# Optimization experiments

Hardware: AMD Instinct MI355X
Metric: run time of the kernel (lower is better)

The kernel has to match this reference:

```python
import jax, jax.numpy as jnp
import numpy as np

EMBED_DIM = 1024
NUM_HEADS = 16
SEQ = 2048
BATCH = 2


def setup_inputs() -> dict:
    key = jax.random.key(0)
    ks = jax.random.split(key, 9)
    E = EMBED_DIM
    gain = 1.0 / np.sqrt(2.0)  # xavier_uniform with gain 1/sqrt(2) (qkv_same_dim)
    limit = gain * np.sqrt(6.0 / (E + E))
    q = jax.random.normal(ks[0], (SEQ, BATCH, E), dtype=jnp.float32)
    k = jax.random.normal(ks[1], (SEQ, BATCH, E), dtype=jnp.float32)
    v = jax.random.normal(ks[2], (SEQ, BATCH, E), dtype=jnp.float32)
    Wq = jax.random.uniform(ks[3], (E, E), jnp.float32, -limit, limit)
    Wk = jax.random.uniform(ks[4], (E, E), jnp.float32, -limit, limit)
    Wv = jax.random.uniform(ks[5], (E, E), jnp.float32, -limit, limit)
    bq = jnp.zeros((E,), jnp.float32)
    bk = jnp.zeros((E,), jnp.float32)
    bv = jnp.zeros((E,), jnp.float32)
    return {"query": q, "key": k, "value": v,
            "Wq": Wq, "bq": bq, "Wk": Wk, "bk": bk, "Wv": Wv, "bv": bv}


def reference(query, key, value, Wq, bq, Wk, bk, Wv, bv):
    # Base Taylor attention path (norm_taylor=True, do_scale=True, has_out=False).
    L, B, E = query.shape
    H = NUM_HEADS
    hd = E // H
    scaling = E ** (-0.5)  # self.scaling = dim**-0.5, dim == embed_dim

    q = (query @ Wq + bq) * scaling          # (L, B, E)
    k = key @ Wk + bk                         # (S, B, E)
    v = value @ Wv + bv                       # (S, B, E)

    def split_heads(x):
        # (T, B, E) -> (B*H, T, hd)
        T = x.shape[0]
        return x.reshape(T, B * H, hd).transpose(1, 0, 2)

    qh, kh, vh = split_heads(q), split_heads(k), split_heads(v)

    # Taylor expansion of exp(qk) to first order: 1 + q.k
    attn = 1.0 + jnp.einsum('bld,bsd->bls', qh, kh)   # (B*H, L, S)
    attn = attn / attn.sum(axis=-1, keepdims=True)    # row-normalize
    out = jnp.einsum('bls,bsd->bld', attn, vh)        # (B*H, L, hd)
    out = out.transpose(1, 0, 2).reshape(L, B, E)     # (L, B, E)
    return out
```

## Files before the change

kernel.cpp:

```cpp
#include <hip/hip_runtime.h>
#include <hip/hip_bf16.h>

#define L_SEQ 2048
#define BATCH 2
#define ROWS 4096
#define E 1024
#define NH 16
#define HD 64

typedef __attribute__((ext_vector_type(4))) float f32x4;
typedef __attribute__((ext_vector_type(8))) __bf16 bf16x8;

#define SWZ(byt) ((byt) ^ ((((byt) >> 7) & 7) << 4))

__device__ __forceinline__ void gload16(const void* g, void* l) {
    __builtin_amdgcn_global_load_lds((const __attribute__((address_space(1))) void*)g,
                                     (__attribute__((address_space(3))) void*)l,
                                     16, 0, 0);
}

__global__ __launch_bounds__(256) void prep(const float* __restrict__ q,
                                            const float* __restrict__ k,
                                            const float* __restrict__ v,
                                            const float* __restrict__ Wq,
                                            const float* __restrict__ Wk,
                                            const float* __restrict__ Wv,
                                            __bf16* __restrict__ Xb,
                                            __bf16* __restrict__ Wt) {
    const int z = blockIdx.y;
    if (blockIdx.x < 2048) {
        const float* src = (z == 0) ? q : ((z == 1) ? k : v);
        __bf16* dst = Xb + (size_t)z * ROWS * E;
        const size_t i = ((size_t)blockIdx.x * 256 + threadIdx.x) * 8;
        const float4 a = *(const float4*)(src + i);
        const float4 b = *(const float4*)(src + i + 4);
        bf16x8 o;
        o[0] = (__bf16)a.x; o[1] = (__bf16)a.y; o[2] = (__bf16)a.z; o[3] = (__bf16)a.w;
        o[4] = (__bf16)b.x; o[5] = (__bf16)b.y; o[6] = (__bf16)b.z; o[7] = (__bf16)b.w;
        *(bf16x8*)(dst + i) = o;
        return;
    }
    const float* W = (z == 0) ? Wq : ((z == 1) ? Wk : Wv);
    __bf16* dst = Wt + (size_t)z * E * E;
    __shared__ __align__(16) float t[64][65];
    const int tt = blockIdx.x - 2048;
    const int n0 = (tt & 15) * 64, k0 = (tt >> 4) * 64;
    const int r = threadIdx.x >> 2, c4 = threadIdx.x & 3;
#pragma unroll
    for (int j = 0; j < 4; ++j) {
        const float4 vv = *(const float4*)&W[(size_t)(k0 + r) * E + n0 + c4 * 16 + j * 4];
        t[r][c4 * 16 + j * 4 + 0] = vv.x;
        t[r][c4 * 16 + j * 4 + 1] = vv.y;
        t[r][c4 * 16 + j * 4 + 2] = vv.z;
        t[r][c4 * 16 + j * 4 + 3] = vv.w;
    }
    __syncthreads();
    bf16x8 o0, o1;
#pragma unroll
    for (int j = 0; j < 8; ++j) {
        o0[j] = (__bf16)t[c4 * 16 + j][r];
        o1[j] = (__bf16)t[c4 * 16 + 8 + j][r];
    }
    *(bf16x8*)&dst[(size_t)(n0 + r) * E + k0 + c4 * 16] = o0;
    *(bf16x8*)&dst[(size_t)(n0 + r) * E + k0 + c4 * 16 + 8] = o1;
}

__device__ __forceinline__ bf16x8 fragld32(const char* base, int row, int kg) {
    return *(const bf16x8*)(base + row * 64 + ((kg ^ (row & 3)) << 4));
}

__global__ __launch_bounds__(256) void gemm_qkv(const __bf16* __restrict__ Xb,
                                                const __bf16* __restrict__ Wt,
                                                const float* __restrict__ bq,
                                                const float* __restrict__ bk,
                                                const float* __restrict__ bv,
                                                __bf16* __restrict__ Cb) {
    const int z = blockIdx.z;
    const __bf16* A = Xb + (size_t)z * ROWS * E;
    const __bf16* Bm = Wt + (size_t)z * E * E;
    __bf16* C = Cb + (size_t)z * ROWS * E;
    const float* bias = (z == 0) ? bq : ((z == 1) ? bk : bv);
    const float alpha = (z == 0) ? 0.03125f : 1.0f;
    const int m0 = blockIdx.x * 128, n0 = blockIdx.y * 128;
    __shared__ __align__(16) __bf16 lsA[128 * 32];
    __shared__ __align__(16) __bf16 lsB[128 * 32];
    const int tid = threadIdx.x;
    const int ln = tid & 63, wv = tid >> 6;
    const int lr = ln & 15, kg = ln >> 4;
    const int wm = (wv >> 1) * 64, wn = (wv & 1) * 64;
    const int cs = (((ln & 3) ^ ((ln >> 2) & 3)) << 3);
    f32x4 acc[4][4] = {};
    for (int kt = 0; kt < E; kt += 32) {
        __syncthreads();
#pragma unroll
        for (int i = 0; i < 2; ++i) {
            const int idx = i * 256 + tid;
            const int row = idx >> 2;
            gload16(A + (size_t)(m0 + row) * E + kt + cs, &lsA[(i * 256 + wv * 64) * 8]);
            gload16(Bm + (size_t)(n0 + row) * E + kt + cs, &lsB[(i * 256 + wv * 64) * 8]);
        }
        __syncthreads();
        bf16x8 af[4], bfr[4];
#pragma unroll
        for (int mi = 0; mi < 4; ++mi)
            af[mi] = fragld32((const char*)lsA, wm + mi * 16 + lr, kg);
#pragma unroll
        for (int ni = 0; ni < 4; ++ni)
            bfr[ni] = fragld32((const char*)lsB, wn + ni * 16 + lr, kg);
#pragma unroll
        for (int mi = 0; mi < 4; ++mi)
#pragma unroll
            for (int ni = 0; ni < 4; ++ni)
                acc[mi][ni] = __builtin_amdgcn_mfma_f32_16x16x32_bf16(af[mi], bfr[ni], acc[mi][ni], 0, 0, 0);
    }
#pragma unroll
    for (int mi = 0; mi < 4; ++mi)
#pragma unroll
        for (int ni = 0; ni < 4; ++ni) {
            const int col = n0 + wn + ni * 16 + lr;
            const int rbase = m0 + wm + mi * 16 + kg * 4;
            const float bcol = bias[col];
#pragma unroll
            for (int rr = 0; rr < 4; ++rr)
                C[(size_t)(rbase + rr) * E + col] = (__bf16)((acc[mi][ni][rr] + bcol) * alpha);
        }
}

__global__ __launch_bounds__(256) void reduce_kv(const __bf16* __restrict__ Kb,
                                                 const __bf16* __restrict__ Vb,
                                                 float* __restrict__ Mpart,
                                                 float* __restrict__ ksumP,
                                                 float* __restrict__ vsumP) {
    const int bh = blockIdx.x, b = bh >> 4, h = bh & 15;
    const int ts = blockIdx.y;
    const int t0 = ts * 128;
    __shared__ __align__(16) __bf16 sK[128 * 64];
    __shared__ __align__(16) __bf16 sV[128 * 64];
    __shared__ float red_k[4][64];
    __shared__ float red_v[4][64];
    const int tid = threadIdx.x;
    const int lane = tid & 63, wave = tid >> 6;
    const int lr = lane & 15, kg = lane >> 4;

    float vk[8] = {}, vv[8] = {};
    const int d0 = (tid & 7) * 8;
#pragma unroll
    for (int i = 0; i < 4; ++i) {
        const int t = i * 32 + (tid >> 3);
        const size_t g = (size_t)((t0 + t) * 2 + b) * E + h * 64 + d0;
        const bf16x8 kv = *(const bf16x8*)&Kb[g];
        const bf16x8 vvv = *(const bf16x8*)&Vb[g];
        const int lo = (t * 128 + d0 * 2) ^ (wave << 5);
        *(bf16x8*)((char*)sK + lo) = kv;
        *(bf16x8*)((char*)sV + lo) = vvv;
#pragma unroll
        for (int j = 0; j < 8; ++j) { vk[j] += (float)kv[j]; vv[j] += (float)vvv[j]; }
    }
#pragma unroll
    for (int m = 8; m <= 32; m <<= 1)
#pragma unroll
        for (int j = 0; j < 8; ++j) {
            vk[j] += __shfl_xor(vk[j], m, 64);
            vv[j] += __shfl_xor(vv[j], m, 64);
        }
    if (lane < 8)
#pragma unroll
        for (int j = 0; j < 8; ++j) {
            red_k[wave][lane * 8 + j] = vk[j];
            red_v[wave][lane * 8 + j] = vv[j];
        }
    __syncthreads();

    f32x4 acc[4] = {};
#pragma unroll
    for (int kt = 0; kt < 4; ++kt) {
        const int tb = kt * 32;
        bf16x8 afr, bfr[4];
        const char* pv = (const char*)sV + (((tb + kg * 8) * 128 + (wave * 16 + lr) * 2) ^ (kg << 5));
#pragma unroll
        for (int j = 0; j < 8; ++j) afr[j] = *(const __bf16*)(pv + j * 128);
#pragma unroll
        for (int ni = 0; ni < 4; ++ni) {
            const char* pk = (const char*)sK + (((tb + kg * 8) * 128 + (ni * 16 + lr) * 2) ^ (kg << 5));
#pragma unroll
            for (int j = 0; j < 8; ++j) bfr[ni][j] = *(const __bf16*)(pk + j * 128);
        }
#pragma unroll
        for (int ni = 0; ni < 4; ++ni)
            acc[ni] = __builtin_amdgcn_mfma_f32_16x16x32_bf16(afr, bfr[ni], acc[ni], 0, 0, 0);
    }

    float* Mp = Mpart + ((size_t)bh * 16 + ts) * 4096;
#pragma unroll
    for (int ni = 0; ni < 4; ++ni)
#pragma unroll
        for (int rr = 0; rr < 4; ++rr)
            Mp[(wave * 16 + kg * 4 + rr) * 64 + ni * 16 + lr] = acc[ni][rr];
    if (tid < 64)
        ksumP[(bh * 16 + ts) * 64 + tid] = red_k[0][tid] + red_k[1][tid] + red_k[2][tid] + red_k[3][tid];
    else if (tid < 128) {
        const int d = tid - 64;
        vsumP[(bh * 16 + ts) * 64 + d] = red_v[0][d] + red_v[1][d] + red_v[2][d] + red_v[3][d];
    }
}

__global__ __launch_bounds__(256) void combine_m(const float* __restrict__ Mpart,
                                                 const float* __restrict__ ksumP,
                                                 const float* __restrict__ vsumP,
                                                 float* __restrict__ Mt,
                                                 float* __restrict__ ksum,
                                                 float* __restrict__ vsum) {
    const int blk = blockIdx.x, tid = threadIdx.x;
    if (blk < 256) {
        const int e2 = (blk * 256 + tid) * 2;
        const int bh = e2 >> 12, r = e2 & 4095;
        const float* src = Mpart + (size_t)bh * 16 * 4096 + r;
        float s0 = 0.f, s1 = 0.f;
#pragma unroll
        for (int ts = 0; ts < 16; ++ts) {
            s0 += src[ts * 4096];
            s1 += src[ts * 4096 + 1];
        }
        Mt[(size_t)bh * 4096 + r] = s0;
        Mt[(size_t)bh * 4096 + r + 1] = s1;
    } else if (blk < 264) {
        const int idx = (blk - 256) * 256 + tid;
        const int bh = idx >> 6, d = idx & 63;
        float s = 0.f;
#pragma unroll
        for (int ts = 0; ts < 16; ++ts) s += ksumP[bh * 1024 + ts * 64 + d];
        ksum[idx] = s;
    } else {
        const int idx = (blk - 264) * 256 + tid;
        const int bh = idx >> 6, d = idx & 63;
        float s = 0.f;
#pragma unroll
        for (int ts = 0; ts < 16; ++ts) s += vsumP[bh * 1024 + ts * 64 + d];
        vsum[idx] = s;
    }
}

__global__ __launch_bounds__(256) void taylor_out(const __bf16* __restrict__ Qb,
                                                  const float* __restrict__ Mt,
                                                  const float* __restrict__ ksum,
                                                  const float* __restrict__ vsum,
                                                  float* __restrict__ out) {
    const int b = blockIdx.y;
    const int lblk = blockIdx.x * 16;
    const int tid = threadIdx.x, lane = tid & 63, wave = tid >> 6;
    const int lr = lane & 15, kg = lane >> 4;
    __shared__ __align__(16) __bf16 sM[4][4096];
    for (int hh = 0; hh < 4; ++hh) {
        __syncthreads();
#pragma unroll
        for (int i = 0; i < 8; ++i) {
            const int idx = i * 256 + tid;
            const int hseg = idx >> 9, rem = idx & 511;
            const float* src = &Mt[(size_t)(b * 16 + hseg * 4 + hh) * 4096 + rem * 8];
            const float4 mA = *(const float4*)src;
            const float4 mB = *(const float4*)(src + 4);
            bf16x8 o;
            o[0] = (__bf16)mA.x; o[1] = (__bf16)mA.y; o[2] = (__bf16)mA.z; o[3] = (__bf16)mA.w;
            o[4] = (__bf16)mB.x; o[5] = (__bf16)mB.y; o[6] = (__bf16)mB.z; o[7] = (__bf16)mB.w;
            *(bf16x8*)((char*)&sM[hseg][0] + SWZ(rem * 16)) = o;
        }
        __syncthreads();
        const int h = wave * 4 + hh;
        const int bh = b * 16 + h;
        const int rA = (lblk + lr) * 2 + b;
        const bf16x8 a0 = *(const bf16x8*)&Qb[(size_t)rA * E + h * 64 + kg * 8];
        const bf16x8 a1 = *(const bf16x8*)&Qb[(size_t)rA * E + h * 64 + 32 + kg * 8];
        float p = 0.f;
        const float* ks = &ksum[bh * 64];
#pragma unroll
        for (int j = 0; j < 8; ++j)
            p += (float)a0[j] * ks[kg * 8 + j] + (float)a1[j] * ks[32 + kg * 8 + j];
        p += __shfl_xor(p, 16, 64);
        p += __shfl_xor(p, 32, 64);
        const float Z = 2048.0f + p;
        f32x4 acc[4] = {};
#pragma unroll
        for (int ni = 0; ni < 4; ++ni) {
            const int byt0 = (ni * 16 + lr) * 128 + kg * 16;
            const bf16x8 b0 = *(const bf16x8*)((const char*)&sM[wave][0] + SWZ(byt0));
            const bf16x8 b1 = *(const bf16x8*)((const char*)&sM[wave][0] + SWZ(byt0 + 64));
            acc[ni] = __builtin_amdgcn_mfma_f32_16x16x32_bf16(a0, b0, acc[ni], 0, 0, 0);
            acc[ni] = __builtin_amdgcn_mfma_f32_16x16x32_bf16(a1, b1, acc[ni], 0, 0, 0);
        }
        float invZ[4];
#pragma unroll
        for (int rr = 0; rr < 4; ++rr) invZ[rr] = 1.0f / __shfl(Z, kg * 4 + rr, 64);
        const float* vs = &vsum[bh * 64];
#pragma unroll
        for (int ni = 0; ni < 4; ++ni)
#pragma unroll
            for (int rr = 0; rr < 4; ++rr) {
                const int l_out = lblk + kg * 4 + rr;
                out[(size_t)(l_out * 2 + b) * E + h * 64 + ni * 16 + lr] =
                    (vs[ni * 16 + lr] + acc[ni][rr]) * invZ[rr];
            }
    }
}

extern "C" void kernel_launch(void* const* d_in, const int* in_sizes, int n_in,
                              void* d_out, int out_size, void* d_ws, size_t ws_size,
                              hipStream_t stream) {
    const float* q  = (const float*)d_in[0];
    const float* k  = (const float*)d_in[1];
    const float* v  = (const float*)d_in[2];
    const float* Wq = (const float*)d_in[3];
    const float* bq = (const float*)d_in[4];
    const float* Wk = (const float*)d_in[5];
    const float* bk = (const float*)d_in[6];
    const float* Wv = (const float*)d_in[7];
    const float* bv = (const float*)d_in[8];
    float* out = (float*)d_out;
    char* w = (char*)d_ws;
    __bf16* Xb = (__bf16*)(w);
    __bf16* Wt = (__bf16*)(w + 25165824);
    __bf16* Cb = (__bf16*)(w + 31457280);
    float* Mt   = (float*)(w + 56623104);
    float* ksum = (float*)(w + 57147392);
    float* vsum = (float*)(w + 57155584);
    float* Mpart = (float*)(w);
    float* ksumP = (float*)(w + 8388608);
    float* vsumP = (float*)(w + 8519680);

    prep<<<dim3(2304, 3), 256, 0, stream>>>(q, k, v, Wq, Wk, Wv, Xb, Wt);
    gemm_qkv<<<dim3(32, 8, 3), 256, 0, stream>>>(Xb, Wt, bq, bk, bv, Cb);
    reduce_kv<<<dim3(32, 16), 256, 0, stream>>>(Cb + (size_t)ROWS * E,
                                                Cb + 2 * (size_t)ROWS * E, Mpart, ksumP, vsumP);
    combine_m<<<272, 256, 0, stream>>>(Mpart, ksumP, vsumP, Mt, ksum, vsum);
    taylor_out<<<dim3(128, 2), 256, 0, stream>>>(Cb, Mt, ksum, vsum, out);
}
```

Before: 77.94 us.

## Fuse fp32-to-bf16 activation conversion into QKV GEMM tile loads

Removes the separate pass that converted the q/k/v activations to bf16. The GEMM now loads fp32 tiles straight into LDS with a new swizzle and converts to bf16 when building fragments. This drops a 48MB fp32 read plus a 24MB bf16 write-and-reread round trip. In exchange the GEMM reads twice as many A bytes per tile from global memory, uses double the LDS for A, and does the conversion inside the inner loop, repeated by every N-block.

```diff
diff --git a/kernel.cpp b/kernel.cpp
--- a/kernel.cpp
+++ b/kernel.cpp
@@ -19,32 +19,15 @@
                                      16, 0, 0);
 }
 
-__global__ __launch_bounds__(256) void prep(const float* __restrict__ q,
-                                            const float* __restrict__ k,
-                                            const float* __restrict__ v,
-                                            const float* __restrict__ Wq,
-                                            const float* __restrict__ Wk,
-                                            const float* __restrict__ Wv,
-                                            __bf16* __restrict__ Xb,
-                                            __bf16* __restrict__ Wt) {
-    const int z = blockIdx.y;
-    if (blockIdx.x < 2048) {
-        const float* src = (z == 0) ? q : ((z == 1) ? k : v);
-        __bf16* dst = Xb + (size_t)z * ROWS * E;
-        const size_t i = ((size_t)blockIdx.x * 256 + threadIdx.x) * 8;
-        const float4 a = *(const float4*)(src + i);
-        const float4 b = *(const float4*)(src + i + 4);
-        bf16x8 o;
-        o[0] = (__bf16)a.x; o[1] = (__bf16)a.y; o[2] = (__bf16)a.z; o[3] = (__bf16)a.w;
-        o[4] = (__bf16)b.x; o[5] = (__bf16)b.y; o[6] = (__bf16)b.z; o[7] = (__bf16)b.w;
-        *(bf16x8*)(dst + i) = o;
-        return;
-    }
+__global__ __launch_bounds__(256) void prep_w(const float* __restrict__ Wq,
+                                              const float* __restrict__ Wk,
+                                              const float* __restrict__ Wv,
+                                              __bf16* __restrict__ Wt) {
+    const int z = blockIdx.z;
     const float* W = (z == 0) ? Wq : ((z == 1) ? Wk : Wv);
     __bf16* dst = Wt + (size_t)z * E * E;
     __shared__ __align__(16) float t[64][65];
-    const int tt = blockIdx.x - 2048;
-    const int n0 = (tt & 15) * 64, k0 = (tt >> 4) * 64;
+    const int n0 = blockIdx.x * 64, k0 = blockIdx.y * 64;
     const int r = threadIdx.x >> 2, c4 = threadIdx.x & 3;
 #pragma unroll
     for (int j = 0; j < 4; ++j) {
@@ -65,48 +48,61 @@
     *(bf16x8*)&dst[(size_t)(n0 + r) * E + k0 + c4 * 16 + 8] = o1;
 }
 
-__device__ __forceinline__ bf16x8 fragld32(const char* base, int row, int kg) {
-    return *(const bf16x8*)(base + row * 64 + ((kg ^ (row & 3)) << 4));
-}
-
-__global__ __launch_bounds__(256) void gemm_qkv(const __bf16* __restrict__ Xb,
+__global__ __launch_bounds__(256) void gemm_qkv(const float* __restrict__ xq,
+                                                const float* __restrict__ xk,
+                                                const float* __restrict__ xv,
                                                 const __bf16* __restrict__ Wt,
                                                 const float* __restrict__ bq,
                                                 const float* __restrict__ bk,
                                                 const float* __restrict__ bv,
                                                 __bf16* __restrict__ Cb) {
     const int z = blockIdx.z;
-    const __bf16* A = Xb + (size_t)z * ROWS * E;
+    const float* A = (z == 0) ? xq : ((z == 1) ? xk : xv);
     const __bf16* Bm = Wt + (size_t)z * E * E;
     __bf16* C = Cb + (size_t)z * ROWS * E;
     const float* bias = (z == 0) ? bq : ((z == 1) ? bk : bv);
     const float alpha = (z == 0) ? 0.03125f : 1.0f;
     const int m0 = blockIdx.x * 128, n0 = blockIdx.y * 128;
-    __shared__ __align__(16) __bf16 lsA[128 * 32];
+    __shared__ __align__(16) float lsA[128 * 32];
     __shared__ __align__(16) __bf16 lsB[128 * 32];
     const int tid = threadIdx.x;
     const int ln = tid & 63, wv = tid >> 6;
     const int lr = ln & 15, kg = ln >> 4;
     const int wm = (wv >> 1) * 64, wn = (wv & 1) * 64;
-    const int cs = (((ln & 3) ^ ((ln >> 2) & 3)) << 3);
+    const int csA = (((ln & 7) ^ (ln >> 3)) << 2);
+    const int csB = (((ln & 3) ^ ((tid >> 2) & 3)) << 3);
     f32x4 acc[4][4] = {};
     for (int kt = 0; kt < E; kt += 32) {
         __syncthreads();
 #pragma unroll
+        for (int i = 0; i < 4; ++i) {
+            const int S = i * 256 + tid;
+            const int row = S >> 3;
+            gload16(A + (size_t)(m0 + row) * E + kt + csA, (char*)lsA + S * 16);
+        }
+#pragma unroll
         for (int i = 0; i < 2; ++i) {
             const int idx = i * 256 + tid;
             const int row = idx >> 2;
-            gload16(A + (size_t)(m0 + row) * E + kt + cs, &lsA[(i * 256 + wv * 64) * 8]);
-            gload16(Bm + (size_t)(n0 + row) * E + kt + cs, &lsB[(i * 256 + wv * 64) * 8]);
+            gload16(Bm + (size_t)(n0 + row) * E + kt + csB, &lsB[(i * 256 + wv * 64) * 8]);
         }
         __syncthreads();
         bf16x8 af[4], bfr[4];
 #pragma unroll
-        for (int mi = 0; mi < 4; ++mi)
-            af[mi] = fragld32((const char*)lsA, wm + mi * 16 + lr, kg);
-#pragma unroll
-        for (int ni = 0; ni < 4; ++ni)
-            bfr[ni] = fragld32((const char*)lsB, wn + ni * 16 + lr, kg);
+        for (int mi = 0; mi < 4; ++mi) {
+            const int r = wm + mi * 16 + lr;
+            const f32x4 lo = *(const f32x4*)((const char*)lsA + r * 128 + (((2 * kg) ^ (r & 7)) << 4));
+            const f32x4 hi = *(const f32x4*)((const char*)lsA + r * 128 + (((2 * kg + 1) ^ (r & 7)) << 4));
+            af[mi][0] = (__bf16)lo[0]; af[mi][1] = (__bf16)lo[1];
+            af[mi][2] = (__bf16)lo[2]; af[mi][3] = (__bf16)lo[3];
+            af[mi][4] = (__bf16)hi[0]; af[mi][5] = (__bf16)hi[1];
+            af[mi][6] = (__bf16)hi[2]; af[mi][7] = (__bf16)hi[3];
+        }
+#pragma unroll
+        for (int ni = 0; ni < 4; ++ni) {
+            const int r = wn + ni * 16 + lr;
+            bfr[ni] = *(const bf16x8*)((const char*)lsB + r * 64 + ((kg ^ (r & 3)) << 4));
+        }
 #pragma unroll
         for (int mi = 0; mi < 4; ++mi)
 #pragma unroll
@@ -316,18 +312,17 @@
     const float* bv = (const float*)d_in[8];
     float* out = (float*)d_out;
     char* w = (char*)d_ws;
-    __bf16* Xb = (__bf16*)(w);
-    __bf16* Wt = (__bf16*)(w + 25165824);
-    __bf16* Cb = (__bf16*)(w + 31457280);
-    float* Mt   = (float*)(w + 56623104);
-    float* ksum = (float*)(w + 57147392);
-    float* vsum = (float*)(w + 57155584);
-    float* Mpart = (float*)(w);
-    float* ksumP = (float*)(w + 8388608);
-    float* vsumP = (float*)(w + 8519680);
-
-    prep<<<dim3(2304, 3), 256, 0, stream>>>(q, k, v, Wq, Wk, Wv, Xb, Wt);
-    gemm_qkv<<<dim3(32, 8, 3), 256, 0, stream>>>(Xb, Wt, bq, bk, bv, Cb);
+    __bf16* Wt = (__bf16*)(w);
+    __bf16* Cb = (__bf16*)(w + 6291456);
+    float* Mt    = (float*)(w + 31457280);
+    float* ksum  = (float*)(w + 31981568);
+    float* vsum  = (float*)(w + 31989760);
+    float* Mpart = (float*)(w + 31997952);
+    float* ksumP = (float*)(w + 40386560);
+    float* vsumP = (float*)(w + 40517632);
+
+    prep_w<<<dim3(16, 16, 3), 256, 0, stream>>>(Wq, Wk, Wv, Wt);
+    gemm_qkv<<<dim3(32, 8, 3), 256, 0, stream>>>(q, k, v, Wt, bq, bk, bv, Cb);
     reduce_kv<<<dim3(32, 16), 256, 0, stream>>>(Cb + (size_t)ROWS * E,
                                                 Cb + 2 * (size_t)ROWS * E, Mpart, ksumP, vsumP);
     combine_m<<<272, 256, 0, stream>>>(Mpart, ksumP, vsumP, Mt, ksum, vsum);
```

After: 73.56 us. 1.06x faster.

## Triple-buffer QKV GEMM LDS tiles with async global-to-LDS prefetch

Applied to the files above, without the earlier changes.

Replaces the single-buffered QKV projection GEMM with a three-slot LDS ring. Tiles are prefetched two iterations ahead through direct global-to-LDS loads, with vmcnt waits and a single barrier per k-step, so memory latency overlaps the MFMA work. It also raises wave priority around the MFMA block. The cost is three times the LDS footprint, which may lower occupancy. The old gemm_qkv is rewritten too but left unused, and its prefetch loads the wrong tile (T instead of T+2), which would give wrong results if it were called.

```diff
diff --git a/kernel.cpp b/kernel.cpp
--- a/kernel.cpp
+++ b/kernel.cpp
@@ -65,10 +65,6 @@
     *(bf16x8*)&dst[(size_t)(n0 + r) * E + k0 + c4 * 16 + 8] = o1;
 }
 
-__device__ __forceinline__ bf16x8 fragld32(const char* base, int row, int kg) {
-    return *(const bf16x8*)(base + row * 64 + ((kg ^ (row & 3)) << 4));
-}
-
 __global__ __launch_bounds__(256) void gemm_qkv(const __bf16* __restrict__ Xb,
                                                 const __bf16* __restrict__ Wt,
                                                 const float* __restrict__ bq,
@@ -82,37 +78,147 @@
     const float* bias = (z == 0) ? bq : ((z == 1) ? bk : bv);
     const float alpha = (z == 0) ? 0.03125f : 1.0f;
     const int m0 = blockIdx.x * 128, n0 = blockIdx.y * 128;
-    __shared__ __align__(16) __bf16 lsA[128 * 32];
-    __shared__ __align__(16) __bf16 lsB[128 * 32];
+    __shared__ __align__(16) __bf16 lsA[3][128 * 32];
+    __shared__ __align__(16) __bf16 lsB[3][128 * 32];
     const int tid = threadIdx.x;
     const int ln = tid & 63, wv = tid >> 6;
     const int lr = ln & 15, kg = ln >> 4;
     const int wm = (wv >> 1) * 64, wn = (wv & 1) * 64;
-    const int cs = (((ln & 3) ^ ((ln >> 2) & 3)) << 3);
+    const int cs = (((ln & 3) ^ ((tid >> 2) & 3)) << 3);
+
+#define STAGE(T_, slot_)                                                          \
+    {                                                                             \
+        const int kt_ = (T_) * 32;                                                \
+        _Pragma("unroll") for (int i = 0; i < 2; ++i) {                           \
+            const int idx = i * 256 + tid;                                        \
+            const int row = idx >> 2;                                             \
+            gload16(A + (size_t)(m0 + row) * E + kt_ + cs,                        \
+                    (char*)lsA[slot_] + idx * 16);                                \
+        }                                                                         \
+        _Pragma("unroll") for (int i = 0; i < 2; ++i) {                           \
+            const int idx = i * 256 + tid;                                        \
+            const int row = idx >> 2;                                             \
+            gload16(Bm + (size_t)(n0 + row) * E + kt_ + cs,                       \
+                    (char*)lsB[slot_] + idx * 16);                                \
+        }                                                                         \
+    }
+
+    STAGE(0, 0);
+    STAGE(1, 1);
+    asm volatile("s_waitcnt vmcnt(4)" ::: "memory");
+    __builtin_amdgcn_s_barrier();
+
     f32x4 acc[4][4] = {};
-    for (int kt = 0; kt < E; kt += 32) {
-        __syncthreads();
-#pragma unroll
-        for (int i = 0; i < 2; ++i) {
-            const int idx = i * 256 + tid;
-            const int row = idx >> 2;
-            gload16(A + (size_t)(m0 + row) * E + kt + cs, &lsA[(i * 256 + wv * 64) * 8]);
-            gload16(Bm + (size_t)(n0 + row) * E + kt + cs, &lsB[(i * 256 + wv * 64) * 8]);
-        }
-        __syncthreads();
+    for (int T = 0; T < 32; ++T) {
+        const int cur = T % 3;
+        if (T <= 29) { const int nxt = (T + 2) % 3; STAGE(T,  nxt); }
         bf16x8 af[4], bfr[4];
 #pragma unroll
-        for (int mi = 0; mi < 4; ++mi)
-            af[mi] = fragld32((const char*)lsA, wm + mi * 16 + lr, kg);
-#pragma unroll
-        for (int ni = 0; ni < 4; ++ni)
-            bfr[ni] = fragld32((const char*)lsB, wn + ni * 16 + lr, kg);
+        for (int mi = 0; mi < 4; ++mi) {
+            const int r = wm + mi * 16 + lr;
+            af[mi] = *(const bf16x8*)((const char*)lsA[cur] + r * 64 + ((kg ^ (r & 3)) << 4));
+        }
+#pragma unroll
+        for (int ni = 0; ni < 4; ++ni) {
+            const int r = wn + ni * 16 + lr;
+            bfr[ni] = *(const bf16x8*)((const char*)lsB[cur] + r * 64 + ((kg ^ (r & 3)) << 4));
+        }
+        __builtin_amdgcn_s_setprio(1);
 #pragma unroll
         for (int mi = 0; mi < 4; ++mi)
 #pragma unroll
             for (int ni = 0; ni < 4; ++ni)
                 acc[mi][ni] = __builtin_amdgcn_mfma_f32_16x16x32_bf16(af[mi], bfr[ni], acc[mi][ni], 0, 0, 0);
-    }
+        __builtin_amdgcn_s_setprio(0);
+        if (T <= 29)      { asm volatile("s_waitcnt vmcnt(4)" ::: "memory"); }
+        else if (T == 30) { asm volatile("s_waitcnt vmcnt(0)" ::: "memory"); }
+        if (T <= 30) __builtin_amdgcn_s_barrier();
+    }
+#undef STAGE
+
+#pragma unroll
+    for (int mi = 0; mi < 4; ++mi)
+#pragma unroll
+        for (int ni = 0; ni < 4; ++ni) {
+            const int col = n0 + wn + ni * 16 + lr;
+            const int rbase = m0 + wm + mi * 16 + kg * 4;
+            const float bcol = bias[col];
+#pragma unroll
+            for (int rr = 0; rr < 4; ++rr)
+                C[(size_t)(rbase + rr) * E + col] = (__bf16)((acc[mi][ni][rr] + bcol) * alpha);
+        }
+}
+
+__global__ __launch_bounds__(256) void gemm_qkv2(const __bf16* __restrict__ Xb,
+                                                 const __bf16* __restrict__ Wt,
+                                                 const float* __restrict__ bq,
+                                                 const float* __restrict__ bk,
+                                                 const float* __restrict__ bv,
+                                                 __bf16* __restrict__ Cb) {
+    const int z = blockIdx.z;
+    const __bf16* A = Xb + (size_t)z * ROWS * E;
+    const __bf16* Bm = Wt + (size_t)z * E * E;
+    __bf16* C = Cb + (size_t)z * ROWS * E;
+    const float* bias = (z == 0) ? bq : ((z == 1) ? bk : bv);
+    const float alpha = (z == 0) ? 0.03125f : 1.0f;
+    const int m0 = blockIdx.x * 128, n0 = blockIdx.y * 128;
+    __shared__ __align__(16) __bf16 lsA[3][128 * 32];
+    __shared__ __align__(16) __bf16 lsB[3][128 * 32];
+    const int tid = threadIdx.x;
+    const int ln = tid & 63, wv = tid >> 6;
+    const int lr = ln & 15, kg = ln >> 4;
+    const int wm = (wv >> 1) * 64, wn = (wv & 1) * 64;
+    const int cs = (((ln & 3) ^ ((tid >> 2) & 3)) << 3);
+
+#define STAGE2(KT, slot_)                                                         \
+    {                                                                             \
+        _Pragma("unroll") for (int i = 0; i < 2; ++i) {                           \
+            const int idx = i * 256 + tid;                                        \
+            const int row = idx >> 2;                                             \
+            gload16(A + (size_t)(m0 + row) * E + (KT) + cs,                       \
+                    (char*)lsA[slot_] + idx * 16);                                \
+        }                                                                         \
+        _Pragma("unroll") for (int i = 0; i < 2; ++i) {                           \
+            const int idx = i * 256 + tid;                                        \
+            const int row = idx >> 2;                                             \
+            gload16(Bm + (size_t)(n0 + row) * E + (KT) + cs,                      \
+                    (char*)lsB[slot_] + idx * 16);                                \
+        }                                                                         \
+    }
+
+    STAGE2(0, 0);
+    STAGE2(32, 1);
+    asm volatile("s_waitcnt vmcnt(4)" ::: "memory");
+    __builtin_amdgcn_s_barrier();
+
+    f32x4 acc[4][4] = {};
+    for (int T = 0; T < 32; ++T) {
+        const int cur = T % 3;
+        if (T <= 29) STAGE2((T + 2) * 32, (T + 2) % 3);
+        bf16x8 af[4], bfr[4];
+#pragma unroll
+        for (int mi = 0; mi < 4; ++mi) {
+            const int r = wm + mi * 16 + lr;
+            af[mi] = *(const bf16x8*)((const char*)lsA[cur] + r * 64 + ((kg ^ (r & 3)) << 4));
+        }
+#pragma unroll
+        for (int ni = 0; ni < 4; ++ni) {
+            const int r = wn + ni * 16 + lr;
+            bfr[ni] = *(const bf16x8*)((const char*)lsB[cur] + r * 64 + ((kg ^ (r & 3)) << 4));
+        }
+        __builtin_amdgcn_s_setprio(1);
+#pragma unroll
+        for (int mi = 0; mi < 4; ++mi)
+#pragma unroll
+            for (int ni = 0; ni < 4; ++ni)
+                acc[mi][ni] = __builtin_amdgcn_mfma_f32_16x16x32_bf16(af[mi], bfr[ni], acc[mi][ni], 0, 0, 0);
+        __builtin_amdgcn_s_setprio(0);
+        if (T <= 29)      { asm volatile("s_waitcnt vmcnt(4)" ::: "memory"); }
+        else if (T == 30) { asm volatile("s_waitcnt vmcnt(0)" ::: "memory"); }
+        if (T <= 30) __builtin_amdgcn_s_barrier();
+    }
+#undef STAGE2
+
 #pragma unroll
     for (int mi = 0; mi < 4; ++mi)
 #pragma unroll
@@ -327,7 +433,7 @@
     float* vsumP = (float*)(w + 8519680);
 
     prep<<<dim3(2304, 3), 256, 0, stream>>>(q, k, v, Wq, Wk, Wv, Xb, Wt);
-    gemm_qkv<<<dim3(32, 8, 3), 256, 0, stream>>>(Xb, Wt, bq, bk, bv, Cb);
+    gemm_qkv2<<<dim3(32, 8, 3), 256, 0, stream>>>(Xb, Wt, bq, bk, bv, Cb);
     reduce_kv<<<dim3(32, 16), 256, 0, stream>>>(Cb + (size_t)ROWS * E,
                                                 Cb + 2 * (size_t)ROWS * E, Mpart, ksumP, vsumP);
     combine_m<<<272, 256, 0, stream>>>(Mpart, ksumP, vsumP, Mt, ksum, vsum);
```

Result: no change. 78.24 us (+0.4%).
